# Optimization experiments

Hardware: AMD Instinct MI355X
Metric: run time of the kernel (lower is better)

Reference implementation:

```python
import jax, jax.numpy as jnp
import numpy as np

N, E, EL = 100000, 1600000, 200000
DIN, DH, DOUT = 128, 128, 64


def _glorot(k, fi, fo):
    return jax.random.normal(k, (fi, fo), jnp.float32) * jax.lax.rsqrt(jnp.float32(fi))


def setup_inputs() -> dict:
    key = jax.random.key(0)
    ks = jax.random.split(key, 8)
    x = jax.random.normal(ks[0], (N, DIN), jnp.float32)
    edge_index = jax.random.randint(ks[1], (2, E), 0, N)
    edge_label_index = jax.random.randint(ks[2], (2, EL), 0, N)
    return {
        "x": x,
        "W1": _glorot(ks[3], DIN, DH), "b1": jnp.zeros((DH,), jnp.float32),
        "W2": _glorot(ks[4], DH, DH), "b2": jnp.zeros((DH,), jnp.float32),
        "W3": _glorot(ks[5], DH, DOUT), "b3": jnp.zeros((DOUT,), jnp.float32),
        "edge_index": edge_index,
        "edge_label_index": edge_label_index,
    }


def gcn_conv(x, W, b, src, dst, norm, n):
    # PyG GCNConv: h = x @ W; out[dst] += norm * h[src]; out += b
    h = x @ W
    msg = h[src] * norm[:, None]                       # [E+N, d]
    out = jax.ops.segment_sum(msg, dst, num_segments=n)
    return out + b


def reference(x, W1, b1, W2, b2, W3, b3, edge_index, edge_label_index):
    n = x.shape[0]
    loop = jnp.arange(n, dtype=edge_index.dtype)
    src = jnp.concatenate([edge_index[0], loop])       # self-loops appended
    dst = jnp.concatenate([edge_index[1], loop])
    # symmetric normalization: deg from dst (col), norm = d^-1/2[src] * d^-1/2[dst]
    deg = jax.ops.segment_sum(jnp.ones(dst.shape[0], x.dtype), dst, num_segments=n)
    dis = jnp.where(deg > 0, jax.lax.rsqrt(jnp.maximum(deg, 1.0)), 0.0)
    norm = dis[src] * dis[dst]

    z = jax.nn.relu(gcn_conv(x, W1, b1, src, dst, norm, n))
    z = jax.nn.relu(gcn_conv(z, W2, b2, src, dst, norm, n))
    z = gcn_conv(z, W3, b3, src, dst, norm, n)

    # decode
    hidden = z[edge_label_index[0]] * z[edge_label_index[1]]   # [EL, DOUT]
    logits = hidden.sum(axis=-1)                               # [EL]
    nrm = jnp.maximum(jnp.linalg.norm(hidden, axis=1, keepdims=True), 1e-12)
    hidden_n = hidden / nrm                                    # F.normalize(dim=1)
    return (hidden_n, logits)
```

## Files before the change

kernel.cpp:

```cpp
#include <hip/hip_runtime.h>
#include <hip/hip_bf16.h>

#define DIN 128
#define DH  128
#define DOUT 64

#define BSHIFT 9
#define BNODES 512
#define BCAP   12288
#define CHUNK  4096

typedef __attribute__((ext_vector_type(8))) short short8;
typedef __attribute__((ext_vector_type(4))) float f32x4;

static __device__ __forceinline__ unsigned short f2bf(float f) {
    unsigned int u = __float_as_uint(f);
    u += 0x7FFFu + ((u >> 16) & 1u);
    return (unsigned short)(u >> 16);
}
static __device__ __forceinline__ float bflo(unsigned int p) {
    return __uint_as_float(p << 16);
}
static __device__ __forceinline__ float bfhi(unsigned int p) {
    return __uint_as_float(p & 0xFFFF0000u);
}

__global__ __launch_bounds__(256) void prep_w_kernel(const float* __restrict__ W1,
                                                     const float* __restrict__ W2,
                                                     const float* __restrict__ W3,
                                                     unsigned short* __restrict__ Wt1,
                                                     unsigned short* __restrict__ Wt2,
                                                     unsigned short* __restrict__ Wt3,
                                                     int* __restrict__ gcur) {
    int i = blockIdx.x * 256 + threadIdx.x;
    if (blockIdx.x == 0) gcur[threadIdx.x] = 0;
    if (i < 128 * 128) {
        int n = i >> 7, k = i & 127;
        Wt1[n * 128 + k] = f2bf(W1[k * 128 + n]);
        Wt2[n * 128 + k] = f2bf(W2[k * 128 + n]);
        if (n < 64) Wt3[n * 128 + k] = f2bf(W3[k * 64 + n]);
    }
}

__global__ __launch_bounds__(256) void bin_scatter_kernel(const int* __restrict__ ei, int E,
                                                          int* __restrict__ gcur,
                                                          int* __restrict__ pairs) {
    __shared__ int hist[256];
    __shared__ int base[256];
    int t = threadIdx.x;
    hist[t] = 0;
    __syncthreads();
    int e0 = blockIdx.x * CHUNK;
    int srcs[16], dsts[16], rk[16];
    #pragma unroll
    for (int j = 0; j < 16; j++) {
        int e = e0 + j * 256 + t;
        if (e < E) {
            srcs[j] = ei[e];
            dsts[j] = ei[E + e];
            rk[j] = atomicAdd(&hist[dsts[j] >> BSHIFT], 1);
        } else {
            rk[j] = -1;
        }
    }
    __syncthreads();
    base[t] = (hist[t] > 0) ? atomicAdd(&gcur[t], hist[t]) : 0;
    __syncthreads();
    #pragma unroll
    for (int j = 0; j < 16; j++) {
        if (rk[j] >= 0) {
            int b = dsts[j] >> BSHIFT;
            int dl = dsts[j] & (BNODES - 1);
            pairs[(size_t)b * BCAP + base[b] + rk[j]] = (dl << 17) | srcs[j];
        }
    }
}

__global__ __launch_bounds__(256) void bucket_deg_kernel(const int* __restrict__ pairs,
                                                         const int* __restrict__ gcur,
                                                         int* __restrict__ deg, int n) {
    __shared__ int cnt_l[BNODES];
    int t = threadIdx.x, b = blockIdx.x;
    cnt_l[t] = 0; cnt_l[t + 256] = 0;
    __syncthreads();
    int cnt = gcur[b];
    const int* p = pairs + (size_t)b * BCAP;
    for (int i = t; i < cnt; i += 256) {
        int pk = p[i];
        atomicAdd(&cnt_l[pk >> 17], 1);
    }
    __syncthreads();
    int node = (b << BSHIFT) + t;
    if (node < n) deg[node] = cnt_l[t] + 1;
    node += 256;
    if (node < n) deg[node] = cnt_l[t + 256] + 1;
}

__global__ __launch_bounds__(256) void scan_block_sums(const int* __restrict__ deg,
                                                       int* __restrict__ bsum, int n) {
    __shared__ int s[256];
    int t = threadIdx.x, base = blockIdx.x * 1024;
    int v = 0;
    #pragma unroll
    for (int j = 0; j < 4; j++) {
        int idx = base + t * 4 + j;
        if (idx < n) v += deg[idx];
    }
    s[t] = v; __syncthreads();
    for (int off = 128; off > 0; off >>= 1) {
        if (t < off) s[t] += s[t + off];
        __syncthreads();
    }
    if (t == 0) bsum[blockIdx.x] = s[0];
}

__global__ __launch_bounds__(256) void scan_bsum_kernel(int* __restrict__ bsum, int nb) {
    __shared__ int s[256];
    int t = threadIdx.x;
    s[t] = (t < nb) ? bsum[t] : 0; __syncthreads();
    for (int off = 1; off < 256; off <<= 1) {
        int v = (t >= off) ? s[t - off] : 0;
        __syncthreads();
        s[t] += v;
        __syncthreads();
    }
    if (t < nb) bsum[t] = (t > 0) ? s[t - 1] : 0;
}

__global__ __launch_bounds__(256) void scan_final_kernel(const int* __restrict__ deg,
                                                         const int* __restrict__ bsum_ex,
                                                         int* __restrict__ row_start,
                                                         float* __restrict__ dis,
                                                         int* __restrict__ csr_src, int n) {
    __shared__ int s[256];
    int t = threadIdx.x, base = blockIdx.x * 1024;
    int d[4]; int local = 0;
    #pragma unroll
    for (int j = 0; j < 4; j++) {
        int idx = base + t * 4 + j;
        d[j] = (idx < n) ? deg[idx] : 0;
        local += d[j];
    }
    s[t] = local; __syncthreads();
    for (int off = 1; off < 256; off <<= 1) {
        int v = (t >= off) ? s[t - off] : 0;
        __syncthreads();
        s[t] += v;
        __syncthreads();
    }
    int ex = ((t > 0) ? s[t - 1] : 0) + bsum_ex[blockIdx.x];
    #pragma unroll
    for (int j = 0; j < 4; j++) {
        int idx = base + t * 4 + j;
        if (idx < n) {
            row_start[idx] = ex;
            float di = rsqrtf((float)d[j]);
            dis[idx] = di;
            csr_src[ex] = idx;
            if (idx == n - 1) row_start[n] = ex + d[j];
            ex += d[j];
        }
    }
}

__global__ __launch_bounds__(256) void bucket_fill_kernel(const int* __restrict__ pairs,
                                                          const int* __restrict__ gcur,
                                                          const int* __restrict__ row_start,
                                                          int* __restrict__ csr_src, int n) {
    __shared__ int cur[BNODES];
    int t = threadIdx.x, b = blockIdx.x;
    int node = (b << BSHIFT) + t;
    cur[t] = (node < n) ? row_start[node] + 1 : 0;
    int node2 = node + 256;
    cur[t + 256] = (node2 < n) ? row_start[node2] + 1 : 0;
    __syncthreads();
    int cnt = gcur[b];
    const int* p = pairs + (size_t)b * BCAP;
    for (int i = t; i < cnt; i += 256) {
        int pk = p[i];
        int pos = atomicAdd(&cur[pk >> 17], 1);
        csr_src[pos] = pk & 0x1FFFF;
    }
}

template <int NOUT, bool AFP32>
__global__ __launch_bounds__(256) void gemm_bf16_kernel(const void* __restrict__ Av,
                                                        const unsigned short* __restrict__ Wt,
                                                        const float* __restrict__ dis,
                                                        unsigned short* __restrict__ H, int M) {
    int wave = (blockIdx.x * 256 + threadIdx.x) >> 6;
    int lane = threadIdx.x & 63;
    int m0 = wave << 4;
    if (m0 >= M) return;
    int m = lane & 15, q = lane >> 4;
    constexpr int NT = NOUT / 16;
    f32x4 acc[NT];
    #pragma unroll
    for (int t = 0; t < NT; t++) acc[t] = (f32x4){0.f, 0.f, 0.f, 0.f};
    const short8* Arow = (const short8*)((const unsigned short*)Av + (size_t)(m0 + m) * 128);
    const float*  Arow32 = (const float*)Av + (size_t)(m0 + m) * 128;
    #pragma unroll
    for (int kk = 0; kk < 4; kk++) {
        short8 a;
        if (AFP32) {
            float4 u = *(const float4*)(Arow32 + kk * 32 + q * 8);
            float4 v = *(const float4*)(Arow32 + kk * 32 + q * 8 + 4);
            a[0] = (short)f2bf(u.x); a[1] = (short)f2bf(u.y);
            a[2] = (short)f2bf(u.z); a[3] = (short)f2bf(u.w);
            a[4] = (short)f2bf(v.x); a[5] = (short)f2bf(v.y);
            a[6] = (short)f2bf(v.z); a[7] = (short)f2bf(v.w);
        } else {
            a = Arow[kk * 4 + q];
        }
        #pragma unroll
        for (int t = 0; t < NT; t++) {
            const short8* Bp = (const short8*)(Wt + (size_t)(t * 16 + m) * 128);
            short8 b = Bp[kk * 4 + q];
            acc[t] = __builtin_amdgcn_mfma_f32_16x16x32_bf16(a, b, acc[t], 0, 0, 0);
        }
    }
    float ds[4];
    #pragma unroll
    for (int r = 0; r < 4; r++) ds[r] = dis[m0 + q * 4 + r];
    #pragma unroll
    for (int t = 0; t < NT; t++)
        #pragma unroll
        for (int r = 0; r < 4; r++)
            H[(size_t)(m0 + q * 4 + r) * NOUT + t * 16 + m] = f2bf(acc[t][r] * ds[r]);
}

template <int NOUT>
__global__ __launch_bounds__(256) void agg_gemm_kernel(const unsigned short* __restrict__ H,
                                                       const int* __restrict__ row_start,
                                                       const int* __restrict__ csr_src,
                                                       const float* __restrict__ dis,
                                                       const float* __restrict__ bias,
                                                       const unsigned short* __restrict__ Wt,
                                                       unsigned short* __restrict__ Hout,
                                                       int n) {
    __shared__ unsigned short X[16][128];
    int t = threadIdx.x;
    int g = t >> 4, gl = t & 15;
    int row = blockIdx.x * 16 + g;
    int c = gl * 8;
    float acc[8];
    #pragma unroll
    for (int i = 0; i < 8; i++) acc[i] = 0.f;
    if (row < n) {
        int p0 = row_start[row], p1 = row_start[row + 1];
        int p = p0;
        for (; p + 8 <= p1; p += 8) {
            int e[8];
            #pragma unroll
            for (int u = 0; u < 8; u++) e[u] = csr_src[p + u];
            uint4 h[8];
            #pragma unroll
            for (int u = 0; u < 8; u++) h[u] = *(const uint4*)(H + (size_t)e[u] * 128 + c);
            #pragma unroll
            for (int u = 0; u < 8; u++) {
                acc[0] += bflo(h[u].x); acc[1] += bfhi(h[u].x);
                acc[2] += bflo(h[u].y); acc[3] += bfhi(h[u].y);
                acc[4] += bflo(h[u].z); acc[5] += bfhi(h[u].z);
                acc[6] += bflo(h[u].w); acc[7] += bfhi(h[u].w);
            }
        }
        for (; p + 4 <= p1; p += 4) {
            int e0 = csr_src[p],     e1 = csr_src[p + 1];
            int e2 = csr_src[p + 2], e3 = csr_src[p + 3];
            uint4 h0 = *(const uint4*)(H + (size_t)e0 * 128 + c);
            uint4 h1 = *(const uint4*)(H + (size_t)e1 * 128 + c);
            uint4 h2 = *(const uint4*)(H + (size_t)e2 * 128 + c);
            uint4 h3 = *(const uint4*)(H + (size_t)e3 * 128 + c);
            acc[0] += bflo(h0.x) + bflo(h1.x) + bflo(h2.x) + bflo(h3.x);
            acc[1] += bfhi(h0.x) + bfhi(h1.x) + bfhi(h2.x) + bfhi(h3.x);
            acc[2] += bflo(h0.y) + bflo(h1.y) + bflo(h2.y) + bflo(h3.y);
            acc[3] += bfhi(h0.y) + bfhi(h1.y) + bfhi(h2.y) + bfhi(h3.y);
            acc[4] += bflo(h0.z) + bflo(h1.z) + bflo(h2.z) + bflo(h3.z);
            acc[5] += bfhi(h0.z) + bfhi(h1.z) + bfhi(h2.z) + bfhi(h3.z);
            acc[6] += bflo(h0.w) + bflo(h1.w) + bflo(h2.w) + bflo(h3.w);
            acc[7] += bfhi(h0.w) + bfhi(h1.w) + bfhi(h2.w) + bfhi(h3.w);
        }
        for (; p < p1; p++) {
            int e = csr_src[p];
            uint4 h = *(const uint4*)(H + (size_t)e * 128 + c);
            acc[0] += bflo(h.x); acc[1] += bfhi(h.x);
            acc[2] += bflo(h.y); acc[3] += bfhi(h.y);
            acc[4] += bflo(h.z); acc[5] += bfhi(h.z);
            acc[6] += bflo(h.w); acc[7] += bfhi(h.w);
        }
        float dd = dis[row];
        #pragma unroll
        for (int i = 0; i < 8; i++)
            acc[i] = fmaxf(acc[i] * dd + bias[c + i], 0.f);
    }
    int wv = t >> 6, lane = t & 63;
    int m = lane & 15, q = lane >> 4;
    constexpr int TPW = NOUT / 64;
    short8 bfrag[4][TPW];
    #pragma unroll
    for (int kk = 0; kk < 4; kk++)
        #pragma unroll
        for (int tt = 0; tt < TPW; tt++) {
            const short8* Bp = (const short8*)(Wt + (size_t)((wv * TPW + tt) * 16 + m) * 128);
            bfrag[kk][tt] = Bp[kk * 4 + q];
        }
    int obase = blockIdx.x * 16;
    float dsout[4];
    #pragma unroll
    for (int r = 0; r < 4; r++) {
        int rr = obase + q * 4 + r;
        dsout[r] = (rr < n) ? dis[rr] : 0.f;
    }
    uint4 pk;
    pk.x = ((unsigned int)f2bf(acc[1]) << 16) | f2bf(acc[0]);
    pk.y = ((unsigned int)f2bf(acc[3]) << 16) | f2bf(acc[2]);
    pk.z = ((unsigned int)f2bf(acc[5]) << 16) | f2bf(acc[4]);
    pk.w = ((unsigned int)f2bf(acc[7]) << 16) | f2bf(acc[6]);
    *(uint4*)&X[g][c ^ ((g & 7) << 3)] = pk;
    __syncthreads();
    f32x4 gacc[TPW];
    #pragma unroll
    for (int tt = 0; tt < TPW; tt++) gacc[tt] = (f32x4){0.f, 0.f, 0.f, 0.f};
    #pragma unroll
    for (int kk = 0; kk < 4; kk++) {
        short8 a = *(const short8*)&X[m][(kk * 32 + q * 8) ^ ((m & 7) << 3)];
        #pragma unroll
        for (int tt = 0; tt < TPW; tt++)
            gacc[tt] = __builtin_amdgcn_mfma_f32_16x16x32_bf16(a, bfrag[kk][tt], gacc[tt], 0, 0, 0);
    }
    #pragma unroll
    for (int r = 0; r < 4; r++) {
        int rr = obase + q * 4 + r;
        if (rr < n) {
            #pragma unroll
            for (int tt = 0; tt < TPW; tt++)
                Hout[(size_t)rr * NOUT + (wv * TPW + tt) * 16 + m] = f2bf(gacc[tt][r] * dsout[r]);
        }
    }
}

template <int EPL, bool RELU, bool OUTBF>
__global__ __launch_bounds__(256) void aggregate_kernel(const unsigned short* __restrict__ H,
                                                        const int* __restrict__ row_start,
                                                        const int* __restrict__ csr_src,
                                                        const float* __restrict__ dis,
                                                        const float* __restrict__ bias,
                                                        void* __restrict__ out, int n) {
    constexpr int F = EPL * 16;
    int row = (blockIdx.x * 256 + threadIdx.x) >> 4;
    int gl  = threadIdx.x & 15;
    if (row >= n) return;
    int c = gl * EPL;
    float acc[EPL];
    #pragma unroll
    for (int i = 0; i < EPL; i++) acc[i] = 0.f;
    int p0 = row_start[row], p1 = row_start[row + 1];
    int p = p0;
    for (; p + 8 <= p1; p += 8) {
        int e[8];
        #pragma unroll
        for (int u = 0; u < 8; u++) e[u] = csr_src[p + u];
        if (EPL == 8) {
            uint4 h[8];
            #pragma unroll
            for (int u = 0; u < 8; u++) h[u] = *(const uint4*)(H + (size_t)e[u] * F + c);
            #pragma unroll
            for (int u = 0; u < 8; u++) {
                acc[0] += bflo(h[u].x); acc[1] += bfhi(h[u].x);
                acc[2] += bflo(h[u].y); acc[3] += bfhi(h[u].y);
                acc[4] += bflo(h[u].z); acc[5] += bfhi(h[u].z);
                acc[6] += bflo(h[u].w); acc[7] += bfhi(h[u].w);
            }
        } else {
            uint2 h[8];
            #pragma unroll
            for (int u = 0; u < 8; u++) h[u] = *(const uint2*)(H + (size_t)e[u] * F + c);
            #pragma unroll
            for (int u = 0; u < 8; u++) {
                acc[0] += bflo(h[u].x); acc[1] += bfhi(h[u].x);
                acc[2] += bflo(h[u].y); acc[3] += bfhi(h[u].y);
            }
        }
    }
    for (; p + 4 <= p1; p += 4) {
        int e0 = csr_src[p],     e1 = csr_src[p + 1];
        int e2 = csr_src[p + 2], e3 = csr_src[p + 3];
        if (EPL == 8) {
            uint4 h0 = *(const uint4*)(H + (size_t)e0 * F + c);
            uint4 h1 = *(const uint4*)(H + (size_t)e1 * F + c);
            uint4 h2 = *(const uint4*)(H + (size_t)e2 * F + c);
            uint4 h3 = *(const uint4*)(H + (size_t)e3 * F + c);
            acc[0] += bflo(h0.x) + bflo(h1.x) + bflo(h2.x) + bflo(h3.x);
            acc[1] += bfhi(h0.x) + bfhi(h1.x) + bfhi(h2.x) + bfhi(h3.x);
            acc[2] += bflo(h0.y) + bflo(h1.y) + bflo(h2.y) + bflo(h3.y);
            acc[3] += bfhi(h0.y) + bfhi(h1.y) + bfhi(h2.y) + bfhi(h3.y);
            acc[4] += bflo(h0.z) + bflo(h1.z) + bflo(h2.z) + bflo(h3.z);
            acc[5] += bfhi(h0.z) + bfhi(h1.z) + bfhi(h2.z) + bfhi(h3.z);
            acc[6] += bflo(h0.w) + bflo(h1.w) + bflo(h2.w) + bflo(h3.w);
            acc[7] += bfhi(h0.w) + bfhi(h1.w) + bfhi(h2.w) + bfhi(h3.w);
        } else {
            uint2 h0 = *(const uint2*)(H + (size_t)e0 * F + c);
            uint2 h1 = *(const uint2*)(H + (size_t)e1 * F + c);
            uint2 h2 = *(const uint2*)(H + (size_t)e2 * F + c);
            uint2 h3 = *(const uint2*)(H + (size_t)e3 * F + c);
            acc[0] += bflo(h0.x) + bflo(h1.x) + bflo(h2.x) + bflo(h3.x);
            acc[1] += bfhi(h0.x) + bfhi(h1.x) + bfhi(h2.x) + bfhi(h3.x);
            acc[2] += bflo(h0.y) + bflo(h1.y) + bflo(h2.y) + bflo(h3.y);
            acc[3] += bfhi(h0.y) + bfhi(h1.y) + bfhi(h2.y) + bfhi(h3.y);
        }
    }
    for (; p < p1; p++) {
        int e = csr_src[p];
        if (EPL == 8) {
            uint4 h = *(const uint4*)(H + (size_t)e * F + c);
            acc[0] += bflo(h.x); acc[1] += bfhi(h.x);
            acc[2] += bflo(h.y); acc[3] += bfhi(h.y);
            acc[4] += bflo(h.z); acc[5] += bfhi(h.z);
            acc[6] += bflo(h.w); acc[7] += bfhi(h.w);
        } else {
            uint2 h = *(const uint2*)(H + (size_t)e * F + c);
            acc[0] += bflo(h.x); acc[1] += bfhi(h.x);
            acc[2] += bflo(h.y); acc[3] += bfhi(h.y);
        }
    }
    float dd = dis[row];
    #pragma unroll
    for (int i = 0; i < EPL; i++) {
        acc[i] = acc[i] * dd + bias[c + i];
        if (RELU) acc[i] = fmaxf(acc[i], 0.f);
    }
    if (OUTBF) {
        unsigned short* ob = (unsigned short*)out + (size_t)row * F + c;
        if (EPL == 8) {
            uint4 pk;
            pk.x = ((unsigned int)f2bf(acc[1]) << 16) | f2bf(acc[0]);
            pk.y = ((unsigned int)f2bf(acc[3]) << 16) | f2bf(acc[2]);
            pk.z = ((unsigned int)f2bf(acc[5]) << 16) | f2bf(acc[4]);
            pk.w = ((unsigned int)f2bf(acc[7]) << 16) | f2bf(acc[6]);
            *(uint4*)ob = pk;
        } else {
            uint2 pk;
            pk.x = ((unsigned int)f2bf(acc[1]) << 16) | f2bf(acc[0]);
            pk.y = ((unsigned int)f2bf(acc[3]) << 16) | f2bf(acc[2]);
            *(uint2*)ob = pk;
        }
    } else {
        float* of = (float*)out + (size_t)row * F + c;
        #pragma unroll
        for (int i = 0; i < EPL; i += 4) {
            *(float4*)(of + i) = make_float4(acc[i], acc[i + 1], acc[i + 2], acc[i + 3]);
        }
    }
}

__global__ __launch_bounds__(256) void decode_kernel(const float* __restrict__ Z,
                                                     const int* __restrict__ eli, int EL,
                                                     float* __restrict__ out_h,
                                                     float* __restrict__ out_l) {
    int g  = (blockIdx.x * 256 + threadIdx.x) >> 4;
    int gl = threadIdx.x & 15;
    int q0 = g * 2;
    if (q0 >= EL) return;
    int q1 = q0 + 1;
    bool has1 = q1 < EL;
    int a0 = eli[q0], b0 = eli[EL + q0];
    int a1 = has1 ? eli[q1] : a0;
    int b1 = has1 ? eli[EL + q1] : b0;
    float4 za0 = *(const float4*)(Z + (size_t)a0 * 64 + gl * 4);
    float4 zb0 = *(const float4*)(Z + (size_t)b0 * 64 + gl * 4);
    float4 za1 = *(const float4*)(Z + (size_t)a1 * 64 + gl * 4);
    float4 zb1 = *(const float4*)(Z + (size_t)b1 * 64 + gl * 4);

    float h00 = za0.x * zb0.x, h01 = za0.y * zb0.y, h02 = za0.z * zb0.z, h03 = za0.w * zb0.w;
    float h10 = za1.x * zb1.x, h11 = za1.y * zb1.y, h12 = za1.z * zb1.z, h13 = za1.w * zb1.w;
    float s0  = h00 + h01 + h02 + h03;
    float ss0 = h00 * h00 + h01 * h01 + h02 * h02 + h03 * h03;
    float s1  = h10 + h11 + h12 + h13;
    float ss1 = h10 * h10 + h11 * h11 + h12 * h12 + h13 * h13;
    #pragma unroll
    for (int off = 8; off > 0; off >>= 1) {
        s0  += __shfl_xor(s0, off, 64);
        ss0 += __shfl_xor(ss0, off, 64);
        s1  += __shfl_xor(s1, off, 64);
        ss1 += __shfl_xor(ss1, off, 64);
    }
    float inv0 = 1.0f / fmaxf(sqrtf(ss0), 1e-12f);
    *(float4*)(out_h + (size_t)q0 * 64 + gl * 4) =
        make_float4(h00 * inv0, h01 * inv0, h02 * inv0, h03 * inv0);
    if (gl == 0) out_l[q0] = s0;
    if (has1) {
        float inv1 = 1.0f / fmaxf(sqrtf(ss1), 1e-12f);
        *(float4*)(out_h + (size_t)q1 * 64 + gl * 4) =
            make_float4(h10 * inv1, h11 * inv1, h12 * inv1, h13 * inv1);
        if (gl == 0) out_l[q1] = s1;
    }
}

extern "C" void kernel_launch(void* const* d_in, const int* in_sizes, int n_in,
                              void* d_out, int out_size, void* d_ws, size_t ws_size,
                              hipStream_t stream) {
    const float* x  = (const float*)d_in[0];
    const float* W1 = (const float*)d_in[1];
    const float* b1 = (const float*)d_in[2];
    const float* W2 = (const float*)d_in[3];
    const float* b2 = (const float*)d_in[4];
    const float* W3 = (const float*)d_in[5];
    const float* b3 = (const float*)d_in[6];
    const int* edge_index = (const int*)d_in[7];
    const int* eli        = (const int*)d_in[8];

    const int N  = in_sizes[0] / DIN;
    const int E  = in_sizes[7] / 2;
    const int EL = in_sizes[8] / 2;
    const int NBUCK = (N + BNODES - 1) >> BSHIFT;

    char* w = (char*)d_ws;
    auto alloc = [&](size_t bytes) -> char* {
        char* p = w; w += (bytes + 255) & ~(size_t)255; return p;
    };
    unsigned short* bufA  = (unsigned short*)alloc((size_t)N * DH * 2);
    unsigned short* bufB  = (unsigned short*)alloc((size_t)N * DH * 2);
    float*          Z3    = (float*)alloc((size_t)N * DOUT * 4);
    unsigned short* Wt1   = (unsigned short*)alloc(128 * 128 * 2);
    unsigned short* Wt2   = (unsigned short*)alloc(128 * 128 * 2);
    unsigned short* Wt3   = (unsigned short*)alloc(64 * 128 * 2);
    int*            deg   = (int*)alloc((size_t)N * 4);
    int*            row_start = (int*)alloc((size_t)(N + 1) * 4);
    float*          dis    = (float*)alloc((size_t)N * 4);
    int*            bsum   = (int*)alloc(1024);
    int*            gcur   = (int*)alloc(256 * 4);
    int*            csr_src = (int*)alloc((size_t)(E + N) * 4);
    int*            pairs  = (int*)alloc((size_t)NBUCK * BCAP * 4);

    float* out_h = (float*)d_out;
    float* out_l = out_h + (size_t)EL * DOUT;

    const int NB = (N + 1023) / 1024;

    prep_w_kernel<<<64, 256, 0, stream>>>(W1, W2, W3, Wt1, Wt2, Wt3, gcur);
    bin_scatter_kernel<<<(E + CHUNK - 1) / CHUNK, 256, 0, stream>>>(edge_index, E, gcur, pairs);
    bucket_deg_kernel<<<NBUCK, 256, 0, stream>>>(pairs, gcur, deg, N);
    scan_block_sums<<<NB, 256, 0, stream>>>(deg, bsum, N);
    scan_bsum_kernel<<<1, 256, 0, stream>>>(bsum, NB);
    scan_final_kernel<<<NB, 256, 0, stream>>>(deg, bsum, row_start, dis, csr_src, N);
    bucket_fill_kernel<<<NBUCK, 256, 0, stream>>>(pairs, gcur, row_start, csr_src, N);

    const int gemm_grid = ((N / 16) * 64 + 255) / 256;
    const int fuse_grid = (N + 15) / 16;
    const int agg_grid  = (N * 16 + 255) / 256;

    gemm_bf16_kernel<128, true><<<gemm_grid, 256, 0, stream>>>(x, Wt1, dis, bufA, N);
    agg_gemm_kernel<128><<<fuse_grid, 256, 0, stream>>>(bufA, row_start, csr_src, dis, b1, Wt2, bufB, N);
    agg_gemm_kernel<64><<<fuse_grid, 256, 0, stream>>>(bufB, row_start, csr_src, dis, b2, Wt3, bufA, N);
    aggregate_kernel<4, false, false><<<agg_grid, 256, 0, stream>>>(bufA, row_start, csr_src, dis, b3, Z3, N);
    const int dec_groups = (EL + 1) / 2;
    decode_kernel<<<(dec_groups * 16 + 255) / 256, 256, 0, stream>>>(Z3, eli, EL, out_h, out_l);
}
```

Before: 404.9 us.

## Fuse CSR build into bucket-level scan and single build kernel

Replaces the five-kernel CSR construction (bucket degree count, three-stage node scan, bucket fill) with a single-block scan over bucket totals followed by one 1024-thread-per-bucket kernel. That kernel counts degrees in shared memory, scans them locally, writes row_start, dis and the self-loop entry, then fills csr_src. This removes several launches and the global deg round trip. The bin scatter chunk is also halved to launch more blocks. The trade-off is one large-block kernel over 196 buckets with a serial shared-memory scan.

```diff
diff --git a/kernel.cpp b/kernel.cpp
--- a/kernel.cpp
+++ b/kernel.cpp
@@ -8,7 +8,7 @@
 #define BSHIFT 9
 #define BNODES 512
 #define BCAP   12288
-#define CHUNK  4096
+#define CHUNK  2048
 
 typedef __attribute__((ext_vector_type(8))) short short8;
 typedef __attribute__((ext_vector_type(4))) float f32x4;
@@ -51,9 +51,9 @@
     hist[t] = 0;
     __syncthreads();
     int e0 = blockIdx.x * CHUNK;
-    int srcs[16], dsts[16], rk[16];
-    #pragma unroll
-    for (int j = 0; j < 16; j++) {
+    int srcs[8], dsts[8], rk[8];
+    #pragma unroll
+    for (int j = 0; j < 8; j++) {
         int e = e0 + j * 256 + t;
         if (e < E) {
             srcs[j] = ei[e];
@@ -67,7 +67,7 @@
     base[t] = (hist[t] > 0) ? atomicAdd(&gcur[t], hist[t]) : 0;
     __syncthreads();
     #pragma unroll
-    for (int j = 0; j < 16; j++) {
+    for (int j = 0; j < 8; j++) {
         if (rk[j] >= 0) {
             int b = dsts[j] >> BSHIFT;
             int dl = dsts[j] & (BNODES - 1);
@@ -76,109 +76,75 @@
     }
 }
 
-__global__ __launch_bounds__(256) void bucket_deg_kernel(const int* __restrict__ pairs,
-                                                         const int* __restrict__ gcur,
-                                                         int* __restrict__ deg, int n) {
-    __shared__ int cnt_l[BNODES];
-    int t = threadIdx.x, b = blockIdx.x;
-    cnt_l[t] = 0; cnt_l[t + 256] = 0;
-    __syncthreads();
-    int cnt = gcur[b];
-    const int* p = pairs + (size_t)b * BCAP;
-    for (int i = t; i < cnt; i += 256) {
-        int pk = p[i];
-        atomicAdd(&cnt_l[pk >> 17], 1);
-    }
-    __syncthreads();
-    int node = (b << BSHIFT) + t;
-    if (node < n) deg[node] = cnt_l[t] + 1;
-    node += 256;
-    if (node < n) deg[node] = cnt_l[t + 256] + 1;
-}
-
-__global__ __launch_bounds__(256) void scan_block_sums(const int* __restrict__ deg,
-                                                       int* __restrict__ bsum, int n) {
-    __shared__ int s[256];
-    int t = threadIdx.x, base = blockIdx.x * 1024;
-    int v = 0;
-    #pragma unroll
-    for (int j = 0; j < 4; j++) {
-        int idx = base + t * 4 + j;
-        if (idx < n) v += deg[idx];
-    }
-    s[t] = v; __syncthreads();
-    for (int off = 128; off > 0; off >>= 1) {
-        if (t < off) s[t] += s[t + off];
-        __syncthreads();
-    }
-    if (t == 0) bsum[blockIdx.x] = s[0];
-}
-
-__global__ __launch_bounds__(256) void scan_bsum_kernel(int* __restrict__ bsum, int nb) {
+__global__ __launch_bounds__(256) void scan_buckets_kernel(const int* __restrict__ gcur,
+                                                           int* __restrict__ bucket_base,
+                                                           int nbuck, int n) {
     __shared__ int s[256];
     int t = threadIdx.x;
-    s[t] = (t < nb) ? bsum[t] : 0; __syncthreads();
+    int own = 0;
+    if (t < nbuck) {
+        int lo = t << BSHIFT;
+        int cnt = n - lo;
+        if (cnt > BNODES) cnt = BNODES;
+        if (cnt < 0) cnt = 0;
+        own = gcur[t] + cnt;
+    }
+    s[t] = own;
+    __syncthreads();
     for (int off = 1; off < 256; off <<= 1) {
         int v = (t >= off) ? s[t - off] : 0;
         __syncthreads();
         s[t] += v;
         __syncthreads();
     }
-    if (t < nb) bsum[t] = (t > 0) ? s[t - 1] : 0;
-}
-
-__global__ __launch_bounds__(256) void scan_final_kernel(const int* __restrict__ deg,
-                                                         const int* __restrict__ bsum_ex,
-                                                         int* __restrict__ row_start,
-                                                         float* __restrict__ dis,
-                                                         int* __restrict__ csr_src, int n) {
-    __shared__ int s[256];
-    int t = threadIdx.x, base = blockIdx.x * 1024;
-    int d[4]; int local = 0;
-    #pragma unroll
-    for (int j = 0; j < 4; j++) {
-        int idx = base + t * 4 + j;
-        d[j] = (idx < n) ? deg[idx] : 0;
-        local += d[j];
-    }
-    s[t] = local; __syncthreads();
-    for (int off = 1; off < 256; off <<= 1) {
-        int v = (t >= off) ? s[t - off] : 0;
+    if (t < nbuck) bucket_base[t] = s[t] - own;
+}
+
+__global__ __launch_bounds__(1024) void bucket_build_kernel(const int* __restrict__ pairs,
+                                                            const int* __restrict__ gcur,
+                                                            const int* __restrict__ bucket_base,
+                                                            int* __restrict__ row_start,
+                                                            float* __restrict__ dis,
+                                                            int* __restrict__ csr_src, int n) {
+    __shared__ int cnt[BNODES];
+    __shared__ int snode[BNODES];
+    int t = threadIdx.x, b = blockIdx.x;
+    if (t < BNODES) cnt[t] = 0;
+    __syncthreads();
+    int m = gcur[b];
+    const int* p = pairs + (size_t)b * BCAP;
+    for (int i = t; i < m; i += 1024) {
+        atomicAdd(&cnt[p[i] >> 17], 1);
+    }
+    __syncthreads();
+    if (t < BNODES) {
+        int node = (b << BSHIFT) + t;
+        snode[t] = (node < n) ? cnt[t] + 1 : 0;
+    }
+    __syncthreads();
+    for (int off = 1; off < BNODES; off <<= 1) {
+        int v = (t < BNODES && t >= off) ? snode[t - off] : 0;
         __syncthreads();
-        s[t] += v;
+        if (t < BNODES) snode[t] += v;
         __syncthreads();
     }
-    int ex = ((t > 0) ? s[t - 1] : 0) + bsum_ex[blockIdx.x];
-    #pragma unroll
-    for (int j = 0; j < 4; j++) {
-        int idx = base + t * 4 + j;
-        if (idx < n) {
-            row_start[idx] = ex;
-            float di = rsqrtf((float)d[j]);
-            dis[idx] = di;
-            csr_src[ex] = idx;
-            if (idx == n - 1) row_start[n] = ex + d[j];
-            ex += d[j];
-        }
-    }
-}
-
-__global__ __launch_bounds__(256) void bucket_fill_kernel(const int* __restrict__ pairs,
-                                                          const int* __restrict__ gcur,
-                                                          const int* __restrict__ row_start,
-                                                          int* __restrict__ csr_src, int n) {
-    __shared__ int cur[BNODES];
-    int t = threadIdx.x, b = blockIdx.x;
-    int node = (b << BSHIFT) + t;
-    cur[t] = (node < n) ? row_start[node] + 1 : 0;
-    int node2 = node + 256;
-    cur[t + 256] = (node2 < n) ? row_start[node2] + 1 : 0;
-    __syncthreads();
-    int cnt = gcur[b];
-    const int* p = pairs + (size_t)b * BCAP;
-    for (int i = t; i < cnt; i += 256) {
+    int bbase = bucket_base[b];
+    if (t < BNODES) {
+        int node = (b << BSHIFT) + t;
+        if (node < n) {
+            int deg = cnt[t] + 1;
+            int ex = bbase + snode[t] - deg;
+            row_start[node] = ex;
+            dis[node] = rsqrtf((float)deg);
+            csr_src[ex] = node;
+            cnt[t] = ex + 1;
+            if (node == n - 1) row_start[n] = ex + deg;
+        }
+    }
+    __syncthreads();
+    for (int i = t; i < m; i += 1024) {
         int pk = p[i];
-        int pos = atomicAdd(&cur[pk >> 17], 1);
+        int pos = atomicAdd(&cnt[pk >> 17], 1);
         csr_src[pos] = pk & 0x1FFFF;
     }
 }
@@ -524,26 +490,21 @@
     unsigned short* Wt1   = (unsigned short*)alloc(128 * 128 * 2);
     unsigned short* Wt2   = (unsigned short*)alloc(128 * 128 * 2);
     unsigned short* Wt3   = (unsigned short*)alloc(64 * 128 * 2);
-    int*            deg   = (int*)alloc((size_t)N * 4);
     int*            row_start = (int*)alloc((size_t)(N + 1) * 4);
     float*          dis    = (float*)alloc((size_t)N * 4);
-    int*            bsum   = (int*)alloc(1024);
     int*            gcur   = (int*)alloc(256 * 4);
+    int*            bucket_base = (int*)alloc(256 * 4);
     int*            csr_src = (int*)alloc((size_t)(E + N) * 4);
     int*            pairs  = (int*)alloc((size_t)NBUCK * BCAP * 4);
 
     float* out_h = (float*)d_out;
     float* out_l = out_h + (size_t)EL * DOUT;
 
-    const int NB = (N + 1023) / 1024;
-
     prep_w_kernel<<<64, 256, 0, stream>>>(W1, W2, W3, Wt1, Wt2, Wt3, gcur);
     bin_scatter_kernel<<<(E + CHUNK - 1) / CHUNK, 256, 0, stream>>>(edge_index, E, gcur, pairs);
-    bucket_deg_kernel<<<NBUCK, 256, 0, stream>>>(pairs, gcur, deg, N);
-    scan_block_sums<<<NB, 256, 0, stream>>>(deg, bsum, N);
-    scan_bsum_kernel<<<1, 256, 0, stream>>>(bsum, NB);
-    scan_final_kernel<<<NB, 256, 0, stream>>>(deg, bsum, row_start, dis, csr_src, N);
-    bucket_fill_kernel<<<NBUCK, 256, 0, stream>>>(pairs, gcur, row_start, csr_src, N);
+    scan_buckets_kernel<<<1, 256, 0, stream>>>(gcur, bucket_base, NBUCK, N);
+    bucket_build_kernel<<<NBUCK, 1024, 0, stream>>>(pairs, gcur, bucket_base,
+                                                    row_start, dis, csr_src, N);
 
     const int gemm_grid = ((N / 16) * 64 + 255) / 256;
     const int fuse_grid = (N + 15) / 16;
```

Result: faster. 390.9 us (median of 2 runs) (-3.5%).
